# Optimization experiments

Measured on AMD Instinct MI355X. Metric: run time of the kernel, lower is better.

## Reference

```python
import jax, jax.numpy as jnp
import numpy as np

EPS = 1e-5

def _bn(h, g, b, m, v):
    # inference-mode batchnorm, channel axis = 1
    shape = (1, -1) + (1,) * (h.ndim - 2)
    scale = g.reshape(shape) / jnp.sqrt(v.reshape(shape) + EPS)
    return (h - m.reshape(shape)) * scale + b.reshape(shape)

def setup_inputs() -> dict:
    B, Cin, Cout, N, K = 2, 64, 64, 50000, 16
    key = jax.random.key(0)
    ks = jax.random.split(key, 24)
    def bn_params(i, C):
        g = 1.0 + 0.1 * jax.random.normal(ks[i], (C,), jnp.float32)
        b = 0.1 * jax.random.normal(ks[i + 1], (C,), jnp.float32)
        m = 0.1 * jax.random.normal(ks[i + 2], (C,), jnp.float32)
        v = jax.random.uniform(ks[i + 3], (C,), jnp.float32, 0.5, 1.5)
        return g, b, m, v
    bn0_g, bn0_b, bn0_m, bn0_v = bn_params(0, Cin)
    bn2a_g, bn2a_b, bn2a_m, bn2a_v = bn_params(4, Cin)
    bn2b_g, bn2b_b, bn2b_m, bn2b_v = bn_params(8, Cout)
    x = jax.random.normal(ks[12], (B, Cin, N), jnp.float32)
    neighbors = jax.random.randint(ks[13], (B, K, N), 0, N, jnp.int32)
    w1 = 0.05 * jax.random.normal(ks[14], (Cout, Cin), jnp.float32)
    b1 = 0.05 * jax.random.normal(ks[15], (Cout,), jnp.float32)
    w2a = 0.05 * jax.random.normal(ks[16], (Cout, Cin), jnp.float32)
    w2b = 0.05 * jax.random.normal(ks[17], (Cout, Cout), jnp.float32)
    wf = 0.05 * jax.random.normal(ks[18], (Cout, 2 * Cout), jnp.float32)
    bf = 0.05 * jax.random.normal(ks[19], (Cout,), jnp.float32)
    return {"x": x, "neighbors": neighbors,
            "bn0_g": bn0_g, "bn0_b": bn0_b, "bn0_m": bn0_m, "bn0_v": bn0_v,
            "w1": w1, "b1": b1,
            "bn2a_g": bn2a_g, "bn2a_b": bn2a_b, "bn2a_m": bn2a_m, "bn2a_v": bn2a_v,
            "w2a": w2a,
            "bn2b_g": bn2b_g, "bn2b_b": bn2b_b, "bn2b_m": bn2b_m, "bn2b_v": bn2b_v,
            "w2b": w2b, "wf": wf, "bf": bf}

def reference(x, neighbors, bn0_g, bn0_b, bn0_m, bn0_v, w1, b1,
              bn2a_g, bn2a_b, bn2a_m, bn2a_v, w2a,
              bn2b_g, bn2b_b, bn2b_m, bn2b_v, w2b, wf, bf):
    # x: (B, Cin, N), neighbors: (B, K, N) int indices into N
    xn = _bn(x, bn0_g, bn0_b, bn0_m, bn0_v)                    # BatchNorm1d
    point = jnp.einsum('oc,bcn->bon', w1, xn) + b1[None, :, None]  # conv1 (1x1)
    idx = neighbors[:, 1:, :]                                   # (B, K-1, N); skip self (col 0)
    # gathered[b,c,k,n] = xn[b,c, idx[b,k,n]]
    gathered = jax.vmap(lambda xb, ib: xb[:, ib])(xn, idx)      # (B, C, K-1, N)
    diff = jnp.transpose(gathered, (0, 1, 3, 2)) - xn[:, :, :, None]  # (B, C, N, K-1)
    h = _bn(diff, bn2a_g, bn2a_b, bn2a_m, bn2a_v)               # BatchNorm2d
    h = jnp.einsum('oc,bcnk->bonk', w2a, h)                     # Conv2d 1x1, no bias
    h = jax.nn.relu(_bn(h, bn2b_g, bn2b_b, bn2b_m, bn2b_v))
    h = jnp.einsum('oc,bcnk->bonk', w2b, h)                     # Conv2d 1x1, no bias
    neigh = h.max(axis=-1)                                      # max over K-1 neighbors
    cat = jnp.concatenate([point, neigh], axis=1)               # (B, 2*Cout, N)
    return jnp.einsum('oc,bcn->bon', wf, cat) + bf[None, :, None]
```

## Files before the change

### kernel.cpp

```cpp
#include <hip/hip_runtime.h>
#include <hip/hip_bf16.h>

typedef __bf16 bf16x8 __attribute__((ext_vector_type(8)));
typedef float f32x4 __attribute__((ext_vector_type(4)));

#define NPT 50000

#define OFF_Y    0u
#define OFF_PRM  12800000u
#define OFF_W2   12801024u
#define OFF_WP   12809216u
#define OFF_W2B  12817408u
#define OFF_WN   12825600u
#define OFF_FLAG 12833792u

__global__ __launch_bounds__(256) void precompute_kernel(
    const void* bn0_g, const void* bn0_b, const void* bn0_m, const void* bn0_v,
    const void* w1, const void* b1,
    const void* bn2a_g, const void* bn2a_b, const void* bn2a_m, const void* bn2a_v,
    const void* w2a,
    const void* bn2b_g, const void* bn2b_b, const void* bn2b_m, const void* bn2b_v,
    const void* w2b, const void* wf, const void* bfv,
    float* __restrict__ prm, __bf16* __restrict__ W2bf, __bf16* __restrict__ Wpbf,
    __bf16* __restrict__ W2Bbf, __bf16* __restrict__ Wnbf, int* __restrict__ flagp)
{
    __shared__ __bf16 w1s[4096];
    __shared__ __bf16 wfs[8192];
    __shared__ __bf16 w2as[4096];
    __shared__ float b1s[64], bfs[64], s2a[64], t2a[64], s2b[64], t2b[64];
    __shared__ int sflag;
    int t = threadIdx.x;

    if (t == 0) {
        const unsigned short* u = (const unsigned short*)bn0_v;
        int cnt = 0;
        for (int i = 0; i < 64; ++i) {
            float f = __uint_as_float(((unsigned int)u[i]) << 16);
            if (f > 0.4f && f < 1.6f) cnt++;
        }
        int fv = (cnt >= 60) ? 1 : 0;
        sflag = fv;
        *flagp = fv;
    }
    __syncthreads();
    int fl = sflag;

    if (fl) {
        const __bf16* W1  = (const __bf16*)w1;
        const __bf16* W2A = (const __bf16*)w2a;
        const __bf16* WF  = (const __bf16*)wf;
        const __bf16* W2B = (const __bf16*)w2b;
        for (int i = t; i < 4096; i += 256) { w1s[i] = W1[i]; w2as[i] = W2A[i]; W2Bbf[i] = W2B[i]; }
        for (int i = t; i < 8192; i += 256) wfs[i] = WF[i];
        if (t < 64) {
            float s0 = (float)((const __bf16*)bn0_g)[t] / sqrtf((float)((const __bf16*)bn0_v)[t] + 1e-5f);
            prm[t] = s0;
            prm[64 + t] = (float)((const __bf16*)bn0_b)[t] - (float)((const __bf16*)bn0_m)[t] * s0;
            float sa = (float)((const __bf16*)bn2a_g)[t] / sqrtf((float)((const __bf16*)bn2a_v)[t] + 1e-5f);
            s2a[t] = sa;
            t2a[t] = (float)((const __bf16*)bn2a_b)[t] - (float)((const __bf16*)bn2a_m)[t] * sa;
            float sb = (float)((const __bf16*)bn2b_g)[t] / sqrtf((float)((const __bf16*)bn2b_v)[t] + 1e-5f);
            s2b[t] = sb;
            t2b[t] = (float)((const __bf16*)bn2b_b)[t] - (float)((const __bf16*)bn2b_m)[t] * sb;
            b1s[t] = (float)((const __bf16*)b1)[t];
            bfs[t] = (float)((const __bf16*)bfv)[t];
        }
    } else {
        const float* W1  = (const float*)w1;
        const float* W2A = (const float*)w2a;
        const float* WF  = (const float*)wf;
        const float* W2B = (const float*)w2b;
        for (int i = t; i < 4096; i += 256) { w1s[i] = (__bf16)W1[i]; w2as[i] = (__bf16)W2A[i]; W2Bbf[i] = (__bf16)W2B[i]; }
        for (int i = t; i < 8192; i += 256) wfs[i] = (__bf16)WF[i];
        if (t < 64) {
            float s0 = ((const float*)bn0_g)[t] / sqrtf(((const float*)bn0_v)[t] + 1e-5f);
            prm[t] = s0;
            prm[64 + t] = ((const float*)bn0_b)[t] - ((const float*)bn0_m)[t] * s0;
            float sa = ((const float*)bn2a_g)[t] / sqrtf(((const float*)bn2a_v)[t] + 1e-5f);
            s2a[t] = sa;
            t2a[t] = ((const float*)bn2a_b)[t] - ((const float*)bn2a_m)[t] * sa;
            float sb = ((const float*)bn2b_g)[t] / sqrtf(((const float*)bn2b_v)[t] + 1e-5f);
            s2b[t] = sb;
            t2b[t] = ((const float*)bn2b_b)[t] - ((const float*)bn2b_m)[t] * sb;
            b1s[t] = ((const float*)b1)[t];
            bfs[t] = ((const float*)bfv)[t];
        }
    }
    __syncthreads();

    for (int e = t; e < 4096; e += 256) {
        int o = e >> 6, c = e & 63;
        W2bf[e] = (__bf16)((float)w2as[e] * s2a[c] * s2b[o]);
        Wnbf[e] = wfs[o * 128 + 64 + c];
        float acc = 0.f;
        for (int m = 0; m < 64; ++m)
            acc += (float)wfs[o * 128 + m] * (float)w1s[m * 64 + c];
        Wpbf[e] = (__bf16)acc;
    }
    if (t < 64) {
        float acc = 0.f, accb = 0.f;
        for (int c = 0; c < 64; ++c) {
            acc  += (float)w2as[t * 64 + c] * t2a[c];
            accb += (float)wfs[t * 128 + c] * b1s[c];
        }
        prm[128 + t] = s2b[t] * acc + t2b[t];
        prm[192 + t] = accb + bfs[t];
    }
}

__global__ __launch_bounds__(256) void pass1_kernel(
    const void* x, const float* __restrict__ prm,
    const __bf16* __restrict__ W2bf, __bf16* __restrict__ Y,
    const int* __restrict__ flagp)
{
    __shared__ float xs[64][65];
    int bid = blockIdx.x;
    int b = bid / 782;
    int n0 = (bid % 782) * 64;
    int npts = NPT - n0; if (npts > 64) npts = 64;
    int fl = *flagp;

    if (fl) {
        const __bf16* xb = (const __bf16*)x + (size_t)b * 64 * NPT;
        for (int i = threadIdx.x; i < 4096; i += 256) {
            int c = i >> 6, p = i & 63;
            float v = (p < npts) ? (float)xb[(size_t)c * NPT + n0 + p] : 0.f;
            xs[p][c] = fmaf(v, prm[c], prm[64 + c]);
        }
    } else {
        const float* xb = (const float*)x + (size_t)b * 64 * NPT;
        for (int i = threadIdx.x; i < 4096; i += 256) {
            int c = i >> 6, p = i & 63;
            float v = (p < npts) ? xb[(size_t)c * NPT + n0 + p] : 0.f;
            xs[p][c] = fmaf(v, prm[c], prm[64 + c]);
        }
    }
    __syncthreads();

    int wid = threadIdx.x >> 6, lane = threadIdx.x & 63;
    int pl = (wid << 4) + (lane & 15);
    int hq = lane >> 4;
    int c0 = hq << 3;

    bf16x8 a0, a1;
    #pragma unroll
    for (int i = 0; i < 8; ++i) {
        a0[i] = (__bf16)xs[pl][c0 + i];
        a1[i] = (__bf16)xs[pl][c0 + 32 + i];
    }

    int ob = lane & 15;
    f32x4 accY[4];
    #pragma unroll
    for (int nt = 0; nt < 4; ++nt) {
        bf16x8 w20 = *(const bf16x8*)(W2bf + (ob + 16 * nt) * 64 + c0);
        bf16x8 w21 = *(const bf16x8*)(W2bf + (ob + 16 * nt) * 64 + c0 + 32);
        f32x4 z = {0.f, 0.f, 0.f, 0.f};
        accY[nt] = __builtin_amdgcn_mfma_f32_16x16x32_bf16(a0, w20, z, 0, 0, 0);
        accY[nt] = __builtin_amdgcn_mfma_f32_16x16x32_bf16(a1, w21, accY[nt], 0, 0, 0);
    }

    #pragma unroll
    for (int nt = 0; nt < 4; ++nt) {
        #pragma unroll
        for (int i = 0; i < 4; ++i) {
            int prow = (wid << 4) + (hq << 2) + i;
            if (prow < npts)
                Y[((size_t)b * NPT + n0 + prow) * 64 + ob + 16 * nt] = (__bf16)accY[nt][i];
        }
    }
}

__global__ __launch_bounds__(256) void pass2_kernel(
    const int* __restrict__ nbr, const __bf16* __restrict__ Y,
    const void* x, const float* __restrict__ prm,
    const __bf16* __restrict__ W2Bbf, const __bf16* __restrict__ Wnbf,
    const __bf16* __restrict__ Wpbf, void* out, const int* __restrict__ flagp)
{
    __shared__ float ns[4][16][68];
    int wid = threadIdx.x >> 6, lane = threadIdx.x & 63;
    int gtile = blockIdx.x * 4 + wid;
    if (gtile >= 6250) return;
    int b = gtile / 3125;
    int n0 = (gtile % 3125) << 4;
    int fl = *flagp;

    int mo = lane & 15;
    int hq = lane >> 4;
    int c0 = hq << 3;
    int nglob = n0 + mo;

    bf16x8 wA[4][2];
    #pragma unroll
    for (int mt = 0; mt < 4; ++mt) {
        wA[mt][0] = *(const bf16x8*)(W2Bbf + (mo + 16 * mt) * 64 + c0);
        wA[mt][1] = *(const bf16x8*)(W2Bbf + (mo + 16 * mt) * 64 + c0 + 32);
    }

    const __bf16* yrow = Y + ((size_t)b * NPT + nglob) * 64;
    float mv[2][8];
    #pragma unroll
    for (int ks = 0; ks < 2; ++ks) {
        bf16x8 yn = *(const bf16x8*)(yrow + c0 + 32 * ks);
        #pragma unroll
        for (int i = 0; i < 8; ++i)
            mv[ks][i] = prm[128 + c0 + 32 * ks + i] - (float)yn[i];
    }

    f32x4 vmax[4];
    #pragma unroll
    for (int mt = 0; mt < 4; ++mt) vmax[mt] = {-3.0e38f, -3.0e38f, -3.0e38f, -3.0e38f};

    const int* nb_base = nbr + (size_t)b * 16 * NPT + NPT + nglob;
    #pragma unroll
    for (int k = 0; k < 15; ++k) {
        int j = nb_base[(size_t)k * NPT];
        const __bf16* yj = Y + ((size_t)b * NPT + j) * 64;
        bf16x8 y0 = *(const bf16x8*)(yj + c0);
        bf16x8 y1 = *(const bf16x8*)(yj + c0 + 32);
        bf16x8 t0, t1;
        #pragma unroll
        for (int i = 0; i < 8; ++i) {
            t0[i] = (__bf16)fmaxf((float)y0[i] + mv[0][i], 0.f);
            t1[i] = (__bf16)fmaxf((float)y1[i] + mv[1][i], 0.f);
        }
        #pragma unroll
        for (int mt = 0; mt < 4; ++mt) {
            f32x4 h = {0.f, 0.f, 0.f, 0.f};
            h = __builtin_amdgcn_mfma_f32_16x16x32_bf16(wA[mt][0], t0, h, 0, 0, 0);
            h = __builtin_amdgcn_mfma_f32_16x16x32_bf16(wA[mt][1], t1, h, 0, 0, 0);
            #pragma unroll
            for (int i = 0; i < 4; ++i) vmax[mt][i] = fmaxf(vmax[mt][i], h[i]);
        }
    }

    #pragma unroll
    for (int mt = 0; mt < 4; ++mt)
        #pragma unroll
        for (int i = 0; i < 4; ++i)
            ns[wid][mo][16 * mt + (hq << 2) + i] = vmax[mt][i];

    bf16x8 nb2[2];
    #pragma unroll
    for (int ks = 0; ks < 2; ++ks)
        #pragma unroll
        for (int i = 0; i < 8; ++i)
            nb2[ks][i] = (__bf16)ns[wid][mo][c0 + 32 * ks + i];

    __builtin_amdgcn_sched_barrier(0);

    bf16x8 xnb[2];
    if (fl) {
        const __bf16* xp = (const __bf16*)x;
        #pragma unroll
        for (int ks = 0; ks < 2; ++ks)
            #pragma unroll
            for (int i = 0; i < 8; ++i) {
                int c = c0 + 32 * ks + i;
                float v = (float)xp[((size_t)b * 64 + c) * NPT + nglob];
                xnb[ks][i] = (__bf16)fmaf(v, prm[c], prm[64 + c]);
            }
    } else {
        const float* xp = (const float*)x;
        #pragma unroll
        for (int ks = 0; ks < 2; ++ks)
            #pragma unroll
            for (int i = 0; i < 8; ++i) {
                int c = c0 + 32 * ks + i;
                float v = xp[((size_t)b * 64 + c) * NPT + nglob];
                xnb[ks][i] = (__bf16)fmaf(v, prm[c], prm[64 + c]);
            }
    }

    bf16x8 wN[4][2], wP[4][2];
    #pragma unroll
    for (int mt = 0; mt < 4; ++mt) {
        wN[mt][0] = *(const bf16x8*)(Wnbf + (mo + 16 * mt) * 64 + c0);
        wN[mt][1] = *(const bf16x8*)(Wnbf + (mo + 16 * mt) * 64 + c0 + 32);
        wP[mt][0] = *(const bf16x8*)(Wpbf + (mo + 16 * mt) * 64 + c0);
        wP[mt][1] = *(const bf16x8*)(Wpbf + (mo + 16 * mt) * 64 + c0 + 32);
    }

    f32x4 oacc[4];
    #pragma unroll
    for (int mt = 0; mt < 4; ++mt) {
        f32x4 acc = *(const f32x4*)(prm + 192 + 16 * mt + 4 * hq);
        acc = __builtin_amdgcn_mfma_f32_16x16x32_bf16(wP[mt][0], xnb[0], acc, 0, 0, 0);
        acc = __builtin_amdgcn_mfma_f32_16x16x32_bf16(wP[mt][1], xnb[1], acc, 0, 0, 0);
        acc = __builtin_amdgcn_mfma_f32_16x16x32_bf16(wN[mt][0], nb2[0], acc, 0, 0, 0);
        acc = __builtin_amdgcn_mfma_f32_16x16x32_bf16(wN[mt][1], nb2[1], acc, 0, 0, 0);
        oacc[mt] = acc;
    }

    if (fl) {
        __bf16* ob = (__bf16*)out + (size_t)b * 64 * NPT + n0 + mo;
        #pragma unroll
        for (int mt = 0; mt < 4; ++mt)
            #pragma unroll
            for (int i = 0; i < 4; ++i)
                ob[(size_t)(16 * mt + (hq << 2) + i) * NPT] = (__bf16)oacc[mt][i];
    } else {
        float* ob = (float*)out + (size_t)b * 64 * NPT + n0 + mo;
        #pragma unroll
        for (int mt = 0; mt < 4; ++mt)
            #pragma unroll
            for (int i = 0; i < 4; ++i)
                ob[(size_t)(16 * mt + (hq << 2) + i) * NPT] = oacc[mt][i];
    }
}

extern "C" void kernel_launch(void* const* d_in, const int* in_sizes, int n_in,
                              void* d_out, int out_size, void* d_ws, size_t ws_size,
                              hipStream_t stream) {
    const void* x      = d_in[0];
    const int*  nbr    = (const int*)d_in[1];

    char* ws = (char*)d_ws;
    __bf16* Y     = (__bf16*)(ws + OFF_Y);
    float*  prm   = (float*)(ws + OFF_PRM);
    __bf16* W2bf  = (__bf16*)(ws + OFF_W2);
    __bf16* Wpbf  = (__bf16*)(ws + OFF_WP);
    __bf16* W2Bbf = (__bf16*)(ws + OFF_W2B);
    __bf16* Wnbf  = (__bf16*)(ws + OFF_WN);
    int*    flagp = (int*)(ws + OFF_FLAG);

    precompute_kernel<<<1, 256, 0, stream>>>(
        d_in[2], d_in[3], d_in[4], d_in[5], d_in[6], d_in[7],
        d_in[8], d_in[9], d_in[10], d_in[11], d_in[12],
        d_in[13], d_in[14], d_in[15], d_in[16], d_in[17], d_in[18], d_in[19],
        prm, W2bf, Wpbf, W2Bbf, Wnbf, flagp);

    pass1_kernel<<<1564, 256, 0, stream>>>(x, prm, W2bf, Y, flagp);

    pass2_kernel<<<1563, 256, 0, stream>>>(nbr, Y, x, prm, W2Bbf, Wnbf, Wpbf, d_out, flagp);
}
```

Before: 211.2 us.

## Split neighbor gather across two waves per tile and batch gather loads

Each 16-point tile is now handled by two waves, each covering half of the 15 neighbors; the halves overlap at k=7, which is harmless for a max. The two partial maxima are combined through shared memory after a __syncthreads, and each wave then computes half of the output channel tiles. All neighbor indices and gathered Y rows are loaded up front so several random gathers are in flight at once, hiding gather latency. The cost is more registers, a block-wide barrier, redundant per-point setup in both waves, and twice as many blocks.

After: 199.5 us. 5.5% less time.

```diff
diff --git a/kernel.cpp b/kernel.cpp
--- a/kernel.cpp
+++ b/kernel.cpp
@@ -177,10 +177,10 @@
     const __bf16* __restrict__ W2Bbf, const __bf16* __restrict__ Wnbf,
     const __bf16* __restrict__ Wpbf, void* out, const int* __restrict__ flagp)
 {
-    __shared__ float ns[4][16][68];
+    __shared__ float ns[2][2][16][69];
     int wid = threadIdx.x >> 6, lane = threadIdx.x & 63;
-    int gtile = blockIdx.x * 4 + wid;
-    if (gtile >= 6250) return;
+    int tile = wid >> 1, h = wid & 1;
+    int gtile = blockIdx.x * 2 + tile;
     int b = gtile / 3125;
     int n0 = (gtile % 3125) << 4;
     int fl = *flagp;
@@ -207,30 +207,40 @@
             mv[ks][i] = prm[128 + c0 + 32 * ks + i] - (float)yn[i];
     }
 
+    const int* nb_base = nbr + (size_t)b * 16 * NPT + NPT + nglob;
+    int kbase = h * 7;
+    int j[8];
+    #pragma unroll
+    for (int kk = 0; kk < 8; ++kk)
+        j[kk] = nb_base[(size_t)(kbase + kk) * NPT];
+
+    bf16x8 y0v[8], y1v[8];
+    #pragma unroll
+    for (int kk = 0; kk < 8; ++kk) {
+        const __bf16* yj = Y + ((size_t)b * NPT + j[kk]) * 64;
+        y0v[kk] = *(const bf16x8*)(yj + c0);
+        y1v[kk] = *(const bf16x8*)(yj + c0 + 32);
+    }
+
     f32x4 vmax[4];
     #pragma unroll
     for (int mt = 0; mt < 4; ++mt) vmax[mt] = {-3.0e38f, -3.0e38f, -3.0e38f, -3.0e38f};
 
-    const int* nb_base = nbr + (size_t)b * 16 * NPT + NPT + nglob;
-    #pragma unroll
-    for (int k = 0; k < 15; ++k) {
-        int j = nb_base[(size_t)k * NPT];
-        const __bf16* yj = Y + ((size_t)b * NPT + j) * 64;
-        bf16x8 y0 = *(const bf16x8*)(yj + c0);
-        bf16x8 y1 = *(const bf16x8*)(yj + c0 + 32);
+    #pragma unroll
+    for (int kk = 0; kk < 8; ++kk) {
         bf16x8 t0, t1;
         #pragma unroll
         for (int i = 0; i < 8; ++i) {
-            t0[i] = (__bf16)fmaxf((float)y0[i] + mv[0][i], 0.f);
-            t1[i] = (__bf16)fmaxf((float)y1[i] + mv[1][i], 0.f);
+            t0[i] = (__bf16)fmaxf((float)y0v[kk][i] + mv[0][i], 0.f);
+            t1[i] = (__bf16)fmaxf((float)y1v[kk][i] + mv[1][i], 0.f);
         }
         #pragma unroll
         for (int mt = 0; mt < 4; ++mt) {
-            f32x4 h = {0.f, 0.f, 0.f, 0.f};
-            h = __builtin_amdgcn_mfma_f32_16x16x32_bf16(wA[mt][0], t0, h, 0, 0, 0);
-            h = __builtin_amdgcn_mfma_f32_16x16x32_bf16(wA[mt][1], t1, h, 0, 0, 0);
-            #pragma unroll
-            for (int i = 0; i < 4; ++i) vmax[mt][i] = fmaxf(vmax[mt][i], h[i]);
+            f32x4 hh = {0.f, 0.f, 0.f, 0.f};
+            hh = __builtin_amdgcn_mfma_f32_16x16x32_bf16(wA[mt][0], t0, hh, 0, 0, 0);
+            hh = __builtin_amdgcn_mfma_f32_16x16x32_bf16(wA[mt][1], t1, hh, 0, 0, 0);
+            #pragma unroll
+            for (int i = 0; i < 4; ++i) vmax[mt][i] = fmaxf(vmax[mt][i], hh[i]);
         }
     }
 
@@ -238,14 +248,18 @@
     for (int mt = 0; mt < 4; ++mt)
         #pragma unroll
         for (int i = 0; i < 4; ++i)
-            ns[wid][mo][16 * mt + (hq << 2) + i] = vmax[mt][i];
+            ns[tile][h][mo][16 * mt + (hq << 2) + i] = vmax[mt][i];
+
+    __syncthreads();
 
     bf16x8 nb2[2];
     #pragma unroll
     for (int ks = 0; ks < 2; ++ks)
         #pragma unroll
-        for (int i = 0; i < 8; ++i)
-            nb2[ks][i] = (__bf16)ns[wid][mo][c0 + 32 * ks + i];
+        for (int i = 0; i < 8; ++i) {
+            int c = c0 + 32 * ks + i;
+            nb2[ks][i] = (__bf16)fmaxf(ns[tile][0][mo][c], ns[tile][1][mo][c]);
+        }
 
     __builtin_amdgcn_sched_barrier(0);
 
@@ -272,40 +286,30 @@
             }
     }
 
-    bf16x8 wN[4][2], wP[4][2];
-    #pragma unroll
-    for (int mt = 0; mt < 4; ++mt) {
-        wN[mt][0] = *(const bf16x8*)(Wnbf + (mo + 16 * mt) * 64 + c0);
-        wN[mt][1] = *(const bf16x8*)(Wnbf + (mo + 16 * mt) * 64 + c0 + 32);
-        wP[mt][0] = *(const bf16x8*)(Wpbf + (mo + 16 * mt) * 64 + c0);
-        wP[mt][1] = *(const bf16x8*)(Wpbf + (mo + 16 * mt) * 64 + c0 + 32);
-    }
-
-    f32x4 oacc[4];
-    #pragma unroll
-    for (int mt = 0; mt < 4; ++mt) {
+    #pragma unroll
+    for (int q = 0; q < 2; ++q) {
+        int mt = 2 * h + q;
+        bf16x8 wn0 = *(const bf16x8*)(Wnbf + (mo + 16 * mt) * 64 + c0);
+        bf16x8 wn1 = *(const bf16x8*)(Wnbf + (mo + 16 * mt) * 64 + c0 + 32);
+        bf16x8 wp0 = *(const bf16x8*)(Wpbf + (mo + 16 * mt) * 64 + c0);
+        bf16x8 wp1 = *(const bf16x8*)(Wpbf + (mo + 16 * mt) * 64 + c0 + 32);
         f32x4 acc = *(const f32x4*)(prm + 192 + 16 * mt + 4 * hq);
-        acc = __builtin_amdgcn_mfma_f32_16x16x32_bf16(wP[mt][0], xnb[0], acc, 0, 0, 0);
-        acc = __builtin_amdgcn_mfma_f32_16x16x32_bf16(wP[mt][1], xnb[1], acc, 0, 0, 0);
-        acc = __builtin_amdgcn_mfma_f32_16x16x32_bf16(wN[mt][0], nb2[0], acc, 0, 0, 0);
-        acc = __builtin_amdgcn_mfma_f32_16x16x32_bf16(wN[mt][1], nb2[1], acc, 0, 0, 0);
-        oacc[mt] = acc;
-    }
-
-    if (fl) {
-        __bf16* ob = (__bf16*)out + (size_t)b * 64 * NPT + n0 + mo;
-        #pragma unroll
-        for (int mt = 0; mt < 4; ++mt)
+        acc = __builtin_amdgcn_mfma_f32_16x16x32_bf16(wp0, xnb[0], acc, 0, 0, 0);
+        acc = __builtin_amdgcn_mfma_f32_16x16x32_bf16(wp1, xnb[1], acc, 0, 0, 0);
+        acc = __builtin_amdgcn_mfma_f32_16x16x32_bf16(wn0, nb2[0], acc, 0, 0, 0);
+        acc = __builtin_amdgcn_mfma_f32_16x16x32_bf16(wn1, nb2[1], acc, 0, 0, 0);
+
+        if (fl) {
+            __bf16* ob = (__bf16*)out + (size_t)b * 64 * NPT + n0 + mo;
             #pragma unroll
             for (int i = 0; i < 4; ++i)
-                ob[(size_t)(16 * mt + (hq << 2) + i) * NPT] = (__bf16)oacc[mt][i];
-    } else {
-        float* ob = (float*)out + (size_t)b * 64 * NPT + n0 + mo;
-        #pragma unroll
-        for (int mt = 0; mt < 4; ++mt)
+                ob[(size_t)(16 * mt + (hq << 2) + i) * NPT] = (__bf16)acc[i];
+        } else {
+            float* ob = (float*)out + (size_t)b * 64 * NPT + n0 + mo;
             #pragma unroll
             for (int i = 0; i < 4; ++i)
-                ob[(size_t)(16 * mt + (hq << 2) + i) * NPT] = oacc[mt][i];
+                ob[(size_t)(16 * mt + (hq << 2) + i) * NPT] = acc[i];
+        }
     }
 }
 
@@ -332,5 +336,5 @@
 
     pass1_kernel<<<1564, 256, 0, stream>>>(x, prm, W2bf, Y, flagp);
 
-    pass2_kernel<<<1563, 256, 0, stream>>>(nbr, Y, x, prm, W2Bbf, Wnbf, Wpbf, d_out, flagp);
+    pass2_kernel<<<3125, 256, 0, stream>>>(nbr, Y, x, prm, W2Bbf, Wnbf, Wpbf, d_out, flagp);
 }
```
